# Performance work log

Measured on AMD Instinct MI355X. Metric: run time of the kernel, lower is better.

Reference implementation:

```python
import jax, jax.numpy as jnp
import numpy as np

NEG_SLOPE = 0.2  # PyG GATv2Conv default
TOPK = 10        # hard-coded in original forward


def setup_inputs() -> dict:
    key = jax.random.key(0)
    N, E, D, L = 50000, 640000, 128, 3
    ks = jax.random.split(key, 12)
    s = 1.0 / np.sqrt(D)
    x = jax.random.normal(ks[0], (N, D), jnp.float32)
    edge_index = jax.random.randint(ks[1], (2, E), 0, N, dtype=jnp.int64)
    edge_attributes = jax.random.normal(ks[2], (E, D), jnp.float32)
    # GATv2 per-layer params (heads=1): lin_l (src), lin_r (dst), lin_edge, att, out bias
    Wl = jax.random.normal(ks[3], (L, D, D), jnp.float32) * s
    bl = jnp.zeros((L, D), jnp.float32)
    Wr = jax.random.normal(ks[4], (L, D, D), jnp.float32) * s
    br = jnp.zeros((L, D), jnp.float32)
    We = jax.random.normal(ks[5], (L, D, D), jnp.float32) * s
    att = jax.random.normal(ks[6], (L, D), jnp.float32) * s
    bias = jnp.zeros((L, D), jnp.float32)
    # final Conv1d(D, 1, 1) == linear projection D -> 1 per node
    Wf = jax.random.normal(ks[7], (D, 1), jnp.float32) * s
    bf = jnp.zeros((1,), jnp.float32)
    return {"x": x, "edge_index": edge_index, "edge_attributes": edge_attributes,
            "Wl": Wl, "bl": bl, "Wr": Wr, "br": br, "We": We, "att": att,
            "bias": bias, "Wf": Wf, "bf": bf}


def _gatv2_layer(x, src, dst, ea, N, Wl, bl, Wr, br, We, att, bias):
    xl = x @ Wl + bl            # [N, D] source transform
    xr = x @ Wr + br            # [N, D] target transform
    ee = ea @ We                # [E', D] edge transform (no bias in PyG lin_edge)
    m = jax.nn.leaky_relu(xl[src] + xr[dst] + ee, NEG_SLOPE)  # [E', D]
    logits = m @ att            # [E']
    # per-destination softmax (every node has a self-loop -> no empty segments)
    mx = jax.ops.segment_max(logits, dst, num_segments=N)
    w = jnp.exp(logits - mx[dst])
    den = jax.ops.segment_sum(w, dst, num_segments=N)
    alpha = w / den[dst]
    out = jax.ops.segment_sum(xl[src] * alpha[:, None], dst, num_segments=N)
    return out + bias


def reference(x, edge_index, edge_attributes, Wl, bl, Wr, br, We, att, bias, Wf, bf):
    N, D = x.shape
    src, dst = edge_index[0], edge_index[1]
    loop = jnp.arange(N, dtype=src.dtype)
    # add_self_loops with fill_value='mean': loop attr = mean of incoming edge attrs
    cnt = jax.ops.segment_sum(jnp.ones_like(dst, dtype=x.dtype), dst, num_segments=N)
    loop_attr = jax.ops.segment_sum(edge_attributes, dst, num_segments=N) / jnp.maximum(cnt, 1.0)[:, None]
    src_f = jnp.concatenate([src, loop])
    dst_f = jnp.concatenate([dst, loop])
    ea = jnp.concatenate([edge_attributes, loop_attr], axis=0)
    L = Wl.shape[0]
    for i in range(L):
        x = _gatv2_layer(x, src_f, dst_f, ea, N, Wl[i], bl[i], Wr[i], br[i], We[i], att[i], bias[i])
    scores = (x @ Wf)[:, 0] + bf[0]   # Conv1d(D,1,1): per-node scalar score [N]
    vals, idx = jax.lax.top_k(scores, TOPK)
    return vals, idx
```

## Files before the change

### kernel.cpp

```cpp
#include <hip/hip_runtime.h>
#include <hip/hip_bf16.h>
#include <float.h>

#define DD 128
#define NEG_SLOPE 0.2f
#define TKB 128

typedef __attribute__((ext_vector_type(8))) short bf16x8;
typedef __attribute__((ext_vector_type(4))) float f32x4;

__device__ __forceinline__ float lrelu(float v) {
    return fmaxf(v, 0.0f) + NEG_SLOPE * fminf(v, 0.0f);
}

__device__ __forceinline__ unsigned short f2bf(float f) {
    unsigned u = __float_as_uint(f);
    u += 0x7fff + ((u >> 16) & 1);
    return (unsigned short)(u >> 16);
}
__device__ __forceinline__ float bf2f(unsigned short h) {
    return __uint_as_float(((unsigned)h) << 16);
}


__global__ void k_hist(const int* __restrict__ dst, int E, int* __restrict__ cnt) {
    int i = blockIdx.x * blockDim.x + threadIdx.x;
    if (i < E) atomicAdd(&cnt[dst[i]], 1);
}

__global__ __launch_bounds__(1024) void k_scan(const int* __restrict__ cnt,
                                               int* __restrict__ row_ptr, int N) {
    __shared__ int sums[1024];
    int tid = threadIdx.x;
    int total = N + 1;
    int chunk = (total + 1023) / 1024;
    int lo = tid * chunk;
    int hi = min(lo + chunk, total);
    int s = 0;
    for (int i = lo; i < hi; ++i) s += (i < N) ? (cnt[i] + 1) : 0;
    sums[tid] = s;
    __syncthreads();
    for (int off = 1; off < 1024; off <<= 1) {
        int t = (tid >= off) ? sums[tid - off] : 0;
        __syncthreads();
        sums[tid] += t;
        __syncthreads();
    }
    int run = sums[tid] - s;
    for (int i = lo; i < hi; ++i) {
        row_ptr[i] = run;
        run += (i < N) ? (cnt[i] + 1) : 0;
    }
}

__global__ void k_scatter(const int* __restrict__ dst, int E, int N,
                          const int* __restrict__ row_ptr, int* __restrict__ fill,
                          const int* __restrict__ cnt, int* __restrict__ eids) {
    int i = blockIdx.x * blockDim.x + threadIdx.x;
    int tot = E + N;
    if (i >= tot) return;
    if (i < E) {
        int d = dst[i];
        int p = atomicAdd(&fill[d], 1);
        eids[row_ptr[d] + p] = i;
    } else {
        int n = i - E;
        eids[row_ptr[n] + cnt[n]] = E + n;
    }
}

__global__ void k_sort_rows(const int* __restrict__ row_ptr, int* __restrict__ eids, int N) {
    int n = blockIdx.x * blockDim.x + threadIdx.x;
    if (n >= N) return;
    int s = row_ptr[n], e = row_ptr[n + 1];
    for (int i = s + 1; i < e; ++i) {
        int v = eids[i];
        int j = i - 1;
        while (j >= s && eids[j] > v) { eids[j + 1] = eids[j]; --j; }
        eids[j + 1] = v;
    }
}

__global__ void k_invert(const int* __restrict__ eids, const int* __restrict__ srcArr,
                         int* __restrict__ pos, int* __restrict__ csr_src, int Etot, int E) {
    int p = blockIdx.x * blockDim.x + threadIdx.x;
    if (p >= Etot) return;
    int eid = eids[p];
    pos[eid] = p;
    csr_src[p] = (eid < E) ? srcArr[eid] : (eid - E);
}

__global__ __launch_bounds__(256) void k_ea_pack(const float* __restrict__ ea,
                                                 const int* __restrict__ row_ptr,
                                                 const int* __restrict__ cnt,
                                                 const int* __restrict__ eids,
                                                 unsigned short* __restrict__ eh,
                                                 unsigned short* __restrict__ el,
                                                 int N, int E) {
    int wid = (blockIdx.x * blockDim.x + threadIdx.x) >> 6;
    int lane = threadIdx.x & 63;
    if (wid >= N) return;
    int s = row_ptr[wid];
    int c = cnt[wid];
    float2 acc = make_float2(0.f, 0.f);
    for (int c0 = 0; c0 < c; c0 += 64) {
        int m = min(64, c - c0);
        int eid = 0;
        if (lane < m) eid = eids[s + c0 + lane];
        int p = 0;
        for (; p + 2 <= m; p += 2) {
            int e0 = __shfl(eid, p), e1 = __shfl(eid, p + 1);
            float2 v0 = *reinterpret_cast<const float2*>(ea + (size_t)e0 * DD + 2 * lane);
            float2 v1 = *reinterpret_cast<const float2*>(ea + (size_t)e1 * DD + 2 * lane);
            acc.x += v0.x; acc.y += v0.y;
            acc.x += v1.x; acc.y += v1.y;
            ushort2 h0, l0, h1, l1;
            h0.x = f2bf(v0.x); l0.x = f2bf(v0.x - bf2f(h0.x));
            h0.y = f2bf(v0.y); l0.y = f2bf(v0.y - bf2f(h0.y));
            h1.x = f2bf(v1.x); l1.x = f2bf(v1.x - bf2f(h1.x));
            h1.y = f2bf(v1.y); l1.y = f2bf(v1.y - bf2f(h1.y));
            *reinterpret_cast<ushort2*>(eh + (size_t)e0 * DD + 2 * lane) = h0;
            *reinterpret_cast<ushort2*>(el + (size_t)e0 * DD + 2 * lane) = l0;
            *reinterpret_cast<ushort2*>(eh + (size_t)e1 * DD + 2 * lane) = h1;
            *reinterpret_cast<ushort2*>(el + (size_t)e1 * DD + 2 * lane) = l1;
        }
        for (; p < m; ++p) {
            int e = __shfl(eid, p);
            float2 v = *reinterpret_cast<const float2*>(ea + (size_t)e * DD + 2 * lane);
            acc.x += v.x; acc.y += v.y;
            ushort2 h, l;
            h.x = f2bf(v.x); l.x = f2bf(v.x - bf2f(h.x));
            h.y = f2bf(v.y); l.y = f2bf(v.y - bf2f(h.y));
            *reinterpret_cast<ushort2*>(eh + (size_t)e * DD + 2 * lane) = h;
            *reinterpret_cast<ushort2*>(el + (size_t)e * DD + 2 * lane) = l;
        }
    }
    float inv = 1.0f / fmaxf((float)c, 1.0f);
    float2 o = make_float2(acc.x * inv, acc.y * inv);
    ushort2 h, l;
    h.x = f2bf(o.x); l.x = f2bf(o.x - bf2f(h.x));
    h.y = f2bf(o.y); l.y = f2bf(o.y - bf2f(h.y));
    *reinterpret_cast<ushort2*>(eh + (size_t)(E + wid) * DD + 2 * lane) = h;
    *reinterpret_cast<ushort2*>(el + (size_t)(E + wid) * DD + 2 * lane) = l;
}

__global__ void k_prepack(const float* __restrict__ W, unsigned short* __restrict__ WA, int L) {
    int idx = blockIdx.x * blockDim.x + threadIdx.x;
    int total = L * DD * DD;
    if (idx >= total) return;
    int l = idx >> 14;
    int rem = idx & 16383;
    int k = rem >> 7;
    int j = rem & 127;
    float w = W[(size_t)l * 16384 + (size_t)k * DD + j];
    unsigned short h = f2bf(w);
    unsigned short lo = f2bf(w - bf2f(h));
    int ks = k >> 5, g = (k >> 3) & 3, i = k & 7;
    size_t off = ((size_t)(ks * 4 + g) * DD + j) * 8 + i;
    unsigned short* base = WA + (size_t)l * 32768;
    base[off] = h;
    base[16384 + off] = lo;
}


__global__ __launch_bounds__(512) void k_gemm2(
    const float* __restrict__ X,
    const unsigned short* __restrict__ WAl, const unsigned short* __restrict__ WAr,
    const float* __restrict__ bl, const float* __restrict__ br,
    float* __restrict__ Yl, float* __restrict__ Yr, int N) {

    __shared__ unsigned short WAs[65536];
    {
        const uint4* g1 = reinterpret_cast<const uint4*>(WAl);
        const uint4* g2 = reinterpret_cast<const uint4*>(WAr);
        uint4* l1 = reinterpret_cast<uint4*>(WAs);
        uint4* l2 = reinterpret_cast<uint4*>(WAs + 32768);
        int t = threadIdx.x;
        #pragma unroll
        for (int i = 0; i < 8; ++i) {
            l1[t + i * 512] = g1[t + i * 512];
            l2[t + i * 512] = g2[t + i * 512];
        }
    }
    __syncthreads();

    int tid  = threadIdx.x;
    int lane = tid & 63;
    int wv   = tid >> 6;
    int lc   = lane & 15;
    int g    = lane >> 4;

    int r0 = blockIdx.x * 256 + wv * 32;
    int rv[2]; bool ok[2];
    const float* rp[2];
    #pragma unroll
    for (int nf = 0; nf < 2; ++nf) {
        rv[nf] = r0 + nf * 16 + lc;
        ok[nf] = (rv[nf] < N);
        rp[nf] = X + (size_t)(ok[nf] ? rv[nf] : 0) * DD;
    }

    f32x4 accl[8][2], accr[8][2];
    #pragma unroll
    for (int m = 0; m < 8; ++m)
        #pragma unroll
        for (int n = 0; n < 2; ++n) {
            accl[m][n] = (f32x4){0.f, 0.f, 0.f, 0.f};
            accr[m][n] = (f32x4){0.f, 0.f, 0.f, 0.f};
        }

    float4 pr0[2], pr1[2];
    #pragma unroll
    for (int nf = 0; nf < 2; ++nf) {
        pr0[nf] = *reinterpret_cast<const float4*>(rp[nf] + g * 8);
        pr1[nf] = *reinterpret_cast<const float4*>(rp[nf] + g * 8 + 4);
    }

    #pragma unroll
    for (int ks = 0; ks < 4; ++ks) {
        bf16x8 Bh[2], Bl[2];
        #pragma unroll
        for (int nf = 0; nf < 2; ++nf) {
            float v[8] = {pr0[nf].x, pr0[nf].y, pr0[nf].z, pr0[nf].w,
                          pr1[nf].x, pr1[nf].y, pr1[nf].z, pr1[nf].w};
            #pragma unroll
            for (int i = 0; i < 8; ++i) {
                unsigned short h = f2bf(v[i]);
                Bh[nf][i] = (short)h;
                Bl[nf][i] = (short)f2bf(v[i] - bf2f(h));
            }
        }
        if (ks < 3) {
            int k0n = (ks + 1) * 32 + g * 8;
            #pragma unroll
            for (int nf = 0; nf < 2; ++nf) {
                pr0[nf] = *reinterpret_cast<const float4*>(rp[nf] + k0n);
                pr1[nf] = *reinterpret_cast<const float4*>(rp[nf] + k0n + 4);
            }
        }
        #pragma unroll
        for (int mf = 0; mf < 8; ++mf) {
            int aoff = ((ks * 4 + g) * DD + (mf * 16 + lc)) * 8;
            bf16x8 Ahl = *reinterpret_cast<const bf16x8*>(&WAs[aoff]);
            bf16x8 All = *reinterpret_cast<const bf16x8*>(&WAs[16384 + aoff]);
            bf16x8 Ahr = *reinterpret_cast<const bf16x8*>(&WAs[32768 + aoff]);
            bf16x8 Alr = *reinterpret_cast<const bf16x8*>(&WAs[49152 + aoff]);
            #pragma unroll
            for (int nf = 0; nf < 2; ++nf) {
                accl[mf][nf] = __builtin_amdgcn_mfma_f32_16x16x32_bf16(Ahl, Bh[nf], accl[mf][nf], 0, 0, 0);
                accl[mf][nf] = __builtin_amdgcn_mfma_f32_16x16x32_bf16(All, Bh[nf], accl[mf][nf], 0, 0, 0);
                accl[mf][nf] = __builtin_amdgcn_mfma_f32_16x16x32_bf16(Ahl, Bl[nf], accl[mf][nf], 0, 0, 0);
                accr[mf][nf] = __builtin_amdgcn_mfma_f32_16x16x32_bf16(Ahr, Bh[nf], accr[mf][nf], 0, 0, 0);
                accr[mf][nf] = __builtin_amdgcn_mfma_f32_16x16x32_bf16(Alr, Bh[nf], accr[mf][nf], 0, 0, 0);
                accr[mf][nf] = __builtin_amdgcn_mfma_f32_16x16x32_bf16(Ahr, Bl[nf], accr[mf][nf], 0, 0, 0);
            }
        }
    }

    #pragma unroll
    for (int mf = 0; mf < 8; ++mf) {
        int f0 = mf * 16 + g * 4;
        float4 blv = *reinterpret_cast<const float4*>(bl + f0);
        float4 brv = *reinterpret_cast<const float4*>(br + f0);
        #pragma unroll
        for (int nf = 0; nf < 2; ++nf) {
            if (!ok[nf]) continue;
            float4 o;
            o.x = accl[mf][nf][0] + blv.x;
            o.y = accl[mf][nf][1] + blv.y;
            o.z = accl[mf][nf][2] + blv.z;
            o.w = accl[mf][nf][3] + blv.w;
            *reinterpret_cast<float4*>(Yl + (size_t)rv[nf] * DD + f0) = o;
            o.x = accr[mf][nf][0] + brv.x;
            o.y = accr[mf][nf][1] + brv.y;
            o.z = accr[mf][nf][2] + brv.z;
            o.w = accr[mf][nf][3] + brv.w;
            *reinterpret_cast<float4*>(Yr + (size_t)rv[nf] * DD + f0) = o;
        }
    }
}

__global__ __launch_bounds__(512, 4) void k_edge_mfma(
    const unsigned short* __restrict__ eh, const unsigned short* __restrict__ el,
    const int* __restrict__ srcArr, const int* __restrict__ dstArr,
    const unsigned short* __restrict__ WA, const float* __restrict__ att,
    const float* __restrict__ xl, const float* __restrict__ xr,
    const int* __restrict__ pos, float* __restrict__ wlog, int E, int Etot) {

    __shared__ unsigned short WAs[32768];
    {
        const uint4* gsrc = reinterpret_cast<const uint4*>(WA);
        uint4* ldst = reinterpret_cast<uint4*>(WAs);
        int t = threadIdx.x;
        #pragma unroll
        for (int i = 0; i < 8; ++i) ldst[t + i * 512] = gsrc[t + i * 512];
    }
    __syncthreads();

    int tid  = threadIdx.x;
    int lane = tid & 63;
    int wv   = tid >> 6;
    int lc   = lane & 15;
    int g    = lane >> 4;

    int e = blockIdx.x * 128 + wv * 16 + lc;
    bool ok = (e < Etot);
    int er = ok ? e : 0;
    const unsigned short* bhp = eh + (size_t)er * DD;
    const unsigned short* blp = el + (size_t)er * DD;

    f32x4 acc[8];
    #pragma unroll
    for (int m = 0; m < 8; ++m) acc[m] = (f32x4){0.f, 0.f, 0.f, 0.f};

    #pragma unroll
    for (int ks = 0; ks < 4; ++ks) {
        int k0 = ks * 32 + g * 8;
        bf16x8 Bh = *reinterpret_cast<const bf16x8*>(bhp + k0);
        bf16x8 Bl = *reinterpret_cast<const bf16x8*>(blp + k0);
        #pragma unroll
        for (int mf = 0; mf < 8; ++mf) {
            int aoff = ((ks * 4 + g) * DD + (mf * 16 + lc)) * 8;
            bf16x8 Ah = *reinterpret_cast<const bf16x8*>(&WAs[aoff]);
            bf16x8 Al = *reinterpret_cast<const bf16x8*>(&WAs[16384 + aoff]);
            acc[mf] = __builtin_amdgcn_mfma_f32_16x16x32_bf16(Ah, Bh, acc[mf], 0, 0, 0);
            acc[mf] = __builtin_amdgcn_mfma_f32_16x16x32_bf16(Al, Bh, acc[mf], 0, 0, 0);
            acc[mf] = __builtin_amdgcn_mfma_f32_16x16x32_bf16(Ah, Bl, acc[mf], 0, 0, 0);
        }
    }

    int sn, dn;
    if (e < E)  { sn = srcArr[e]; dn = dstArr[e]; }
    else if (ok){ sn = e - E; dn = e - E; }
    else        { sn = 0; dn = 0; }
    float partial = 0.f;
    #pragma unroll
    for (int mf = 0; mf < 8; ++mf) {
        int f0 = mf * 16 + g * 4;
        float4 attv = *reinterpret_cast<const float4*>(att + f0);
        float4 xlv  = *reinterpret_cast<const float4*>(xl + (size_t)sn * DD + f0);
        float4 xrv  = *reinterpret_cast<const float4*>(xr + (size_t)dn * DD + f0);
        float t0 = acc[mf][0] + xlv.x + xrv.x;
        float t1 = acc[mf][1] + xlv.y + xrv.y;
        float t2 = acc[mf][2] + xlv.z + xrv.z;
        float t3 = acc[mf][3] + xlv.w + xrv.w;
        partial += attv.x * lrelu(t0) + attv.y * lrelu(t1)
                 + attv.z * lrelu(t2) + attv.w * lrelu(t3);
    }
    partial += __shfl_xor(partial, 16);
    partial += __shfl_xor(partial, 32);
    if (lane < 16 && ok) wlog[pos[e]] = partial;
}

__global__ __launch_bounds__(256) void k_sfx_agg(
    const float* __restrict__ wlog, const int* __restrict__ row_ptr,
    const int* __restrict__ csr_src, const float* __restrict__ xl,
    const float* __restrict__ bias, float* __restrict__ xout, int N) {
    int wid = (blockIdx.x * blockDim.x + threadIdx.x) >> 6;
    int lane = threadIdx.x & 63;
    if (wid >= N) return;
    int s = row_ptr[wid], e = row_ptr[wid + 1];
    float mx = -FLT_MAX;
    for (int c0 = s; c0 < e; c0 += 64) {
        float l = (c0 + lane < e) ? wlog[c0 + lane] : -FLT_MAX;
        l = fmaxf(l, __shfl_xor(l, 32));
        l = fmaxf(l, __shfl_xor(l, 16));
        l = fmaxf(l, __shfl_xor(l, 8));
        l = fmaxf(l, __shfl_xor(l, 4));
        l = fmaxf(l, __shfl_xor(l, 2));
        l = fmaxf(l, __shfl_xor(l, 1));
        mx = fmaxf(mx, l);
    }
    float den = 0.f;
    for (int c0 = s; c0 < e; c0 += 64) {
        float w = (c0 + lane < e) ? __expf(wlog[c0 + lane] - mx) : 0.f;
        w += __shfl_xor(w, 32);
        w += __shfl_xor(w, 16);
        w += __shfl_xor(w, 8);
        w += __shfl_xor(w, 4);
        w += __shfl_xor(w, 2);
        w += __shfl_xor(w, 1);
        den += w;
    }
    float inv = 1.0f / den;
    float2 acc = make_float2(0.f, 0.f);
    for (int c0 = s; c0 < e; c0 += 64) {
        int m = min(64, e - c0);
        float av = 0.f; int sv = 0;
        if (lane < m) {
            av = __expf(wlog[c0 + lane] - mx) * inv;
            sv = csr_src[c0 + lane];
        }
        int p = 0;
        for (; p + 4 <= m; p += 4) {
            float a0 = __shfl(av, p),     a1 = __shfl(av, p + 1);
            float a2 = __shfl(av, p + 2), a3 = __shfl(av, p + 3);
            int   r0 = __shfl(sv, p),     r1 = __shfl(sv, p + 1);
            int   r2 = __shfl(sv, p + 2), r3 = __shfl(sv, p + 3);
            float2 v0 = *reinterpret_cast<const float2*>(xl + (size_t)r0 * DD + 2 * lane);
            float2 v1 = *reinterpret_cast<const float2*>(xl + (size_t)r1 * DD + 2 * lane);
            float2 v2 = *reinterpret_cast<const float2*>(xl + (size_t)r2 * DD + 2 * lane);
            float2 v3 = *reinterpret_cast<const float2*>(xl + (size_t)r3 * DD + 2 * lane);
            acc.x += a0 * v0.x; acc.y += a0 * v0.y;
            acc.x += a1 * v1.x; acc.y += a1 * v1.y;
            acc.x += a2 * v2.x; acc.y += a2 * v2.y;
            acc.x += a3 * v3.x; acc.y += a3 * v3.y;
        }
        for (; p < m; ++p) {
            float ap = __shfl(av, p);
            int   rw = __shfl(sv, p);
            float2 v = *reinterpret_cast<const float2*>(xl + (size_t)rw * DD + 2 * lane);
            acc.x += ap * v.x;
            acc.y += ap * v.y;
        }
    }
    float2 bv = *reinterpret_cast<const float2*>(bias + 2 * lane);
    float2 o = make_float2(acc.x + bv.x, acc.y + bv.y);
    *reinterpret_cast<float2*>(xout + (size_t)wid * DD + 2 * lane) = o;
}


__global__ __launch_bounds__(256) void k_scores(const float* __restrict__ X,
                                                const float* __restrict__ Wf,
                                                const float* __restrict__ bf,
                                                float* __restrict__ scores, int N) {
    int gid = blockIdx.x * blockDim.x + threadIdx.x;
    int node = gid >> 6;
    int lane = threadIdx.x & 63;
    if (node >= N) return;
    float2 xv = *reinterpret_cast<const float2*>(&X[(size_t)node * DD + lane * 2]);
    float2 wv = *reinterpret_cast<const float2*>(&Wf[lane * 2]);
    float p = xv.x * wv.x + xv.y * wv.y;
    p += __shfl_xor(p, 32);
    p += __shfl_xor(p, 16);
    p += __shfl_xor(p, 8);
    p += __shfl_xor(p, 4);
    p += __shfl_xor(p, 2);
    p += __shfl_xor(p, 1);
    if (lane == 0) scores[node] = p + bf[0];
}

__device__ __forceinline__ bool tk_better(float a, int ai, float b, int bi) {
    return (a > b) || (a == b && ai < bi);
}

__device__ __forceinline__ void tk_insert(float sv, int si, float* v, int* ix) {
    if (tk_better(sv, si, v[9], ix[9])) {
        v[9] = sv; ix[9] = si;
        #pragma unroll
        for (int j = 9; j > 0; --j) {
            if (tk_better(v[j], ix[j], v[j - 1], ix[j - 1])) {
                float tv = v[j]; v[j] = v[j - 1]; v[j - 1] = tv;
                int ti = ix[j]; ix[j] = ix[j - 1]; ix[j - 1] = ti;
            }
        }
    }
}

__global__ __launch_bounds__(256) void k_topk1(const float* __restrict__ scores, int N,
                                               float* __restrict__ cand_v, int* __restrict__ cand_i) {
    __shared__ float lv[256 * 10];
    __shared__ int li[256 * 10];
    int t = threadIdx.x;
    float v[10]; int ix[10];
    #pragma unroll
    for (int j = 0; j < 10; ++j) { v[j] = -FLT_MAX; ix[j] = 0x7fffffff; }
    for (int i = blockIdx.x * 256 + t; i < N; i += TKB * 256)
        tk_insert(scores[i], i, v, ix);
    #pragma unroll
    for (int j = 0; j < 10; ++j) { lv[t * 10 + j] = v[j]; li[t * 10 + j] = ix[j]; }
    __syncthreads();
    for (int sh = 128; sh >= 1; sh >>= 1) {
        if (t < sh) {
            float bv[10]; int bi[10];
            #pragma unroll
            for (int j = 0; j < 10; ++j) { bv[j] = lv[(t + sh) * 10 + j]; bi[j] = li[(t + sh) * 10 + j]; }
            float mv[10]; int mi[10];
            int i1 = 0, i2 = 0;
            #pragma unroll
            for (int k = 0; k < 10; ++k) {
                if (tk_better(v[i1], ix[i1], bv[i2], bi[i2])) { mv[k] = v[i1]; mi[k] = ix[i1]; ++i1; }
                else { mv[k] = bv[i2]; mi[k] = bi[i2]; ++i2; }
            }
            #pragma unroll
            for (int j = 0; j < 10; ++j) {
                v[j] = mv[j]; ix[j] = mi[j];
                lv[t * 10 + j] = v[j]; li[t * 10 + j] = ix[j];
            }
        }
        __syncthreads();
    }
    if (t == 0) {
        #pragma unroll
        for (int j = 0; j < 10; ++j) {
            cand_v[blockIdx.x * 10 + j] = v[j];
            cand_i[blockIdx.x * 10 + j] = ix[j];
        }
    }
}

__global__ __launch_bounds__(64) void k_topk2(const float* __restrict__ cand_v,
                                              const int* __restrict__ cand_i,
                                              float* __restrict__ out) {
    __shared__ float lv[64 * 10];
    __shared__ int li[64 * 10];
    int t = threadIdx.x;
    float v[10]; int ix[10];
    #pragma unroll
    for (int j = 0; j < 10; ++j) { v[j] = -FLT_MAX; ix[j] = 0x7fffffff; }
    for (int i = t; i < TKB * 10; i += 64)
        tk_insert(cand_v[i], cand_i[i], v, ix);
    #pragma unroll
    for (int j = 0; j < 10; ++j) { lv[t * 10 + j] = v[j]; li[t * 10 + j] = ix[j]; }
    __syncthreads();
    for (int sh = 32; sh >= 1; sh >>= 1) {
        if (t < sh) {
            float bv[10]; int bi[10];
            #pragma unroll
            for (int j = 0; j < 10; ++j) { bv[j] = lv[(t + sh) * 10 + j]; bi[j] = li[(t + sh) * 10 + j]; }
            float mv[10]; int mi[10];
            int i1 = 0, i2 = 0;
            #pragma unroll
            for (int k = 0; k < 10; ++k) {
                if (tk_better(v[i1], ix[i1], bv[i2], bi[i2])) { mv[k] = v[i1]; mi[k] = ix[i1]; ++i1; }
                else { mv[k] = bv[i2]; mi[k] = bi[i2]; ++i2; }
            }
            #pragma unroll
            for (int j = 0; j < 10; ++j) {
                v[j] = mv[j]; ix[j] = mi[j];
                lv[t * 10 + j] = v[j]; li[t * 10 + j] = ix[j];
            }
        }
        __syncthreads();
    }
    if (t == 0) {
        #pragma unroll
        for (int j = 0; j < 10; ++j) {
            out[j] = v[j];
            out[10 + j] = (float)ix[j];
        }
    }
}


static inline size_t alignup(size_t v) { return (v + 255) & ~(size_t)255; }

extern "C" void kernel_launch(void* const* d_in, const int* in_sizes, int n_in,
                              void* d_out, int out_size, void* d_ws, size_t ws_size,
                              hipStream_t stream) {
    const float* x    = (const float*)d_in[0];
    const int*   ei   = (const int*)d_in[1];
    const float* ea   = (const float*)d_in[2];
    const float* Wl   = (const float*)d_in[3];
    const float* bl   = (const float*)d_in[4];
    const float* Wr   = (const float*)d_in[5];
    const float* br   = (const float*)d_in[6];
    const float* We   = (const float*)d_in[7];
    const float* att  = (const float*)d_in[8];
    const float* bias = (const float*)d_in[9];
    const float* Wf   = (const float*)d_in[10];
    const float* bf   = (const float*)d_in[11];

    int N = in_sizes[0] / DD;
    int E = in_sizes[1] / 2;
    int L = in_sizes[3] / (DD * DD);
    int Etot = E + N;
    const int* src = ei;
    const int* dst = ei + E;

    size_t off = 0;
    char* wsb = (char*)d_ws;
    auto carve = [&](size_t bytes) -> void* { void* p = wsb + off; off += alignup(bytes); return p; };
    unsigned short* WAe = (unsigned short*)carve((size_t)L * 32768 * 2);
    unsigned short* WAl = (unsigned short*)carve((size_t)L * 32768 * 2);
    unsigned short* WAr = (unsigned short*)carve((size_t)L * 32768 * 2);
    int*   cnt       = (int*)carve((size_t)N * 4);
    int*   fill      = (int*)carve((size_t)N * 4);
    int*   row_ptr   = (int*)carve((size_t)(N + 1) * 4);
    int*   eids      = (int*)carve((size_t)Etot * 4);
    int*   pos       = (int*)carve((size_t)Etot * 4);
    int*   csr_src   = (int*)carve((size_t)Etot * 4);
    float* wlog      = (float*)carve((size_t)Etot * 4);
    unsigned short* eh = (unsigned short*)carve((size_t)Etot * DD * 2);
    unsigned short* el = (unsigned short*)carve((size_t)Etot * DD * 2);
    float* xl        = (float*)carve((size_t)N * DD * 4);
    float* xr        = (float*)carve((size_t)N * DD * 4);
    float* xa        = (float*)carve((size_t)N * DD * 4);
    float* xb        = (float*)carve((size_t)N * DD * 4);
    float* scoresBuf = (float*)carve((size_t)N * 4);
    float* cand_v    = (float*)carve((size_t)TKB * 10 * 4);
    int*   cand_i    = (int*)carve((size_t)TKB * 10 * 4);
    (void)ws_size; (void)n_in; (void)out_size;

    hipMemsetAsync(cnt, 0, (size_t)N * 4, stream);
    hipMemsetAsync(fill, 0, (size_t)N * 4, stream);

    int ppBlocks = (L * DD * DD + 255) / 256;
    k_prepack<<<ppBlocks, 256, 0, stream>>>(We, WAe, L);
    k_prepack<<<ppBlocks, 256, 0, stream>>>(Wl, WAl, L);
    k_prepack<<<ppBlocks, 256, 0, stream>>>(Wr, WAr, L);
    k_hist<<<(E + 255) / 256, 256, 0, stream>>>(dst, E, cnt);
    k_scan<<<1, 1024, 0, stream>>>(cnt, row_ptr, N);
    k_scatter<<<(Etot + 255) / 256, 256, 0, stream>>>(dst, E, N, row_ptr, fill, cnt, eids);
    k_sort_rows<<<(N + 255) / 256, 256, 0, stream>>>(row_ptr, eids, N);
    k_invert<<<(Etot + 255) / 256, 256, 0, stream>>>(eids, src, pos, csr_src, Etot, E);
    int waveBlocks = (N * 64 + 255) / 256;
    k_ea_pack<<<waveBlocks, 256, 0, stream>>>(ea, row_ptr, cnt, eids, eh, el, N, E);

    const float* xin = x;
    float* xout = xa;
    int gemmBlocks = (N + 255) / 256;
    int edgeBlocks = (Etot + 127) / 128;
    for (int l = 0; l < L; ++l) {
        k_gemm2<<<gemmBlocks, 512, 0, stream>>>(xin, WAl + (size_t)l * 32768, WAr + (size_t)l * 32768,
                                                bl + (size_t)l * DD, br + (size_t)l * DD, xl, xr, N);
        k_edge_mfma<<<edgeBlocks, 512, 0, stream>>>(eh, el, src, dst,
                                                    WAe + (size_t)l * 32768, att + (size_t)l * DD,
                                                    xl, xr, pos, wlog, E, Etot);
        k_sfx_agg<<<waveBlocks, 256, 0, stream>>>(wlog, row_ptr, csr_src, xl,
                                                  bias + (size_t)l * DD, xout, N);
        xin = xout;
        xout = (xout == xa) ? xb : xa;
    }
    k_scores<<<(N + 3) / 4, 256, 0, stream>>>(xin, Wf, bf, scoresBuf, N);
    k_topk1<<<TKB, 256, 0, stream>>>(scoresBuf, N, cand_v, cand_i);
    k_topk2<<<1, 64, 0, stream>>>(cand_v, cand_i, (float*)d_out);
}
```

Measured before the change: 1.284 ms.

## Fuse edge logit MFMA, online softmax, and aggregation into per-node kernel

Edge attributes are now stored in CSR (destination-sorted) order, so each wave can process one destination node's incoming edges in chunks of 16. The edge-transform MFMA, logit, online softmax and weighted aggregation of xl all happen in one persistent kernel. This drops the wlog and pos buffers and the separate softmax/aggregate pass. The cost is wasted MFMA lanes when a node has fewer than 16 edges (about 13 on average here), many shuffles per chunk for the reduction, and lower occupancy from the new launch bounds.

```diff
diff --git a/kernel.cpp b/kernel.cpp
--- a/kernel.cpp
+++ b/kernel.cpp
@@ -81,12 +81,11 @@
     }
 }
 
-__global__ void k_invert(const int* __restrict__ eids, const int* __restrict__ srcArr,
-                         int* __restrict__ pos, int* __restrict__ csr_src, int Etot, int E) {
+__global__ void k_srcmap(const int* __restrict__ eids, const int* __restrict__ srcArr,
+                         int* __restrict__ csr_src, int Etot, int E) {
     int p = blockIdx.x * blockDim.x + threadIdx.x;
     if (p >= Etot) return;
     int eid = eids[p];
-    pos[eid] = p;
     csr_src[p] = (eid < E) ? srcArr[eid] : (eid - E);
 }
 
@@ -96,7 +95,7 @@
                                                  const int* __restrict__ eids,
                                                  unsigned short* __restrict__ eh,
                                                  unsigned short* __restrict__ el,
-                                                 int N, int E) {
+                                                 int N) {
     int wid = (blockIdx.x * blockDim.x + threadIdx.x) >> 6;
     int lane = threadIdx.x & 63;
     if (wid >= N) return;
@@ -104,11 +103,11 @@
     int c = cnt[wid];
     float2 acc = make_float2(0.f, 0.f);
     for (int c0 = 0; c0 < c; c0 += 64) {
-        int m = min(64, c - c0);
+        int mm = min(64, c - c0);
         int eid = 0;
-        if (lane < m) eid = eids[s + c0 + lane];
+        if (lane < mm) eid = eids[s + c0 + lane];
         int p = 0;
-        for (; p + 2 <= m; p += 2) {
+        for (; p + 2 <= mm; p += 2) {
             int e0 = __shfl(eid, p), e1 = __shfl(eid, p + 1);
             float2 v0 = *reinterpret_cast<const float2*>(ea + (size_t)e0 * DD + 2 * lane);
             float2 v1 = *reinterpret_cast<const float2*>(ea + (size_t)e1 * DD + 2 * lane);
@@ -119,20 +118,23 @@
             h0.y = f2bf(v0.y); l0.y = f2bf(v0.y - bf2f(h0.y));
             h1.x = f2bf(v1.x); l1.x = f2bf(v1.x - bf2f(h1.x));
             h1.y = f2bf(v1.y); l1.y = f2bf(v1.y - bf2f(h1.y));
-            *reinterpret_cast<ushort2*>(eh + (size_t)e0 * DD + 2 * lane) = h0;
-            *reinterpret_cast<ushort2*>(el + (size_t)e0 * DD + 2 * lane) = l0;
-            *reinterpret_cast<ushort2*>(eh + (size_t)e1 * DD + 2 * lane) = h1;
-            *reinterpret_cast<ushort2*>(el + (size_t)e1 * DD + 2 * lane) = l1;
-        }
-        for (; p < m; ++p) {
+            size_t r0 = (size_t)(s + c0 + p) * DD + 2 * lane;
+            size_t r1 = (size_t)(s + c0 + p + 1) * DD + 2 * lane;
+            *reinterpret_cast<ushort2*>(eh + r0) = h0;
+            *reinterpret_cast<ushort2*>(el + r0) = l0;
+            *reinterpret_cast<ushort2*>(eh + r1) = h1;
+            *reinterpret_cast<ushort2*>(el + r1) = l1;
+        }
+        for (; p < mm; ++p) {
             int e = __shfl(eid, p);
             float2 v = *reinterpret_cast<const float2*>(ea + (size_t)e * DD + 2 * lane);
             acc.x += v.x; acc.y += v.y;
             ushort2 h, l;
             h.x = f2bf(v.x); l.x = f2bf(v.x - bf2f(h.x));
             h.y = f2bf(v.y); l.y = f2bf(v.y - bf2f(h.y));
-            *reinterpret_cast<ushort2*>(eh + (size_t)e * DD + 2 * lane) = h;
-            *reinterpret_cast<ushort2*>(el + (size_t)e * DD + 2 * lane) = l;
+            size_t ro = (size_t)(s + c0 + p) * DD + 2 * lane;
+            *reinterpret_cast<ushort2*>(eh + ro) = h;
+            *reinterpret_cast<ushort2*>(el + ro) = l;
         }
     }
     float inv = 1.0f / fmaxf((float)c, 1.0f);
@@ -140,8 +142,9 @@
     ushort2 h, l;
     h.x = f2bf(o.x); l.x = f2bf(o.x - bf2f(h.x));
     h.y = f2bf(o.y); l.y = f2bf(o.y - bf2f(h.y));
-    *reinterpret_cast<ushort2*>(eh + (size_t)(E + wid) * DD + 2 * lane) = h;
-    *reinterpret_cast<ushort2*>(el + (size_t)(E + wid) * DD + 2 * lane) = l;
+    size_t ro = (size_t)(s + c) * DD + 2 * lane;
+    *reinterpret_cast<ushort2*>(eh + ro) = h;
+    *reinterpret_cast<ushort2*>(el + ro) = l;
 }
 
 __global__ void k_prepack(const float* __restrict__ W, unsigned short* __restrict__ WA, int L) {
@@ -280,12 +283,13 @@
     }
 }
 
-__global__ __launch_bounds__(512, 4) void k_edge_mfma(
+__global__ __launch_bounds__(512, 2) void k_node_fused(
     const unsigned short* __restrict__ eh, const unsigned short* __restrict__ el,
-    const int* __restrict__ srcArr, const int* __restrict__ dstArr,
+    const int* __restrict__ row_ptr, const int* __restrict__ csr_src,
     const unsigned short* __restrict__ WA, const float* __restrict__ att,
     const float* __restrict__ xl, const float* __restrict__ xr,
-    const int* __restrict__ pos, float* __restrict__ wlog, int E, int Etot) {
+    const float* __restrict__ bias, float* __restrict__ xout,
+    int N, int nodeStride) {
 
     __shared__ unsigned short WAs[32768];
     {
@@ -303,120 +307,113 @@
     int lc   = lane & 15;
     int g    = lane >> 4;
 
-    int e = blockIdx.x * 128 + wv * 16 + lc;
-    bool ok = (e < Etot);
-    int er = ok ? e : 0;
-    const unsigned short* bhp = eh + (size_t)er * DD;
-    const unsigned short* blp = el + (size_t)er * DD;
-
-    f32x4 acc[8];
-    #pragma unroll
-    for (int m = 0; m < 8; ++m) acc[m] = (f32x4){0.f, 0.f, 0.f, 0.f};
-
-    #pragma unroll
-    for (int ks = 0; ks < 4; ++ks) {
-        int k0 = ks * 32 + g * 8;
-        bf16x8 Bh = *reinterpret_cast<const bf16x8*>(bhp + k0);
-        bf16x8 Bl = *reinterpret_cast<const bf16x8*>(blp + k0);
-        #pragma unroll
-        for (int mf = 0; mf < 8; ++mf) {
-            int aoff = ((ks * 4 + g) * DD + (mf * 16 + lc)) * 8;
-            bf16x8 Ah = *reinterpret_cast<const bf16x8*>(&WAs[aoff]);
-            bf16x8 Al = *reinterpret_cast<const bf16x8*>(&WAs[16384 + aoff]);
-            acc[mf] = __builtin_amdgcn_mfma_f32_16x16x32_bf16(Ah, Bh, acc[mf], 0, 0, 0);
-            acc[mf] = __builtin_amdgcn_mfma_f32_16x16x32_bf16(Al, Bh, acc[mf], 0, 0, 0);
-            acc[mf] = __builtin_amdgcn_mfma_f32_16x16x32_bf16(Ah, Bl, acc[mf], 0, 0, 0);
-        }
-    }
-
-    int sn, dn;
-    if (e < E)  { sn = srcArr[e]; dn = dstArr[e]; }
-    else if (ok){ sn = e - E; dn = e - E; }
-    else        { sn = 0; dn = 0; }
-    float partial = 0.f;
-    #pragma unroll
-    for (int mf = 0; mf < 8; ++mf) {
-        int f0 = mf * 16 + g * 4;
-        float4 attv = *reinterpret_cast<const float4*>(att + f0);
-        float4 xlv  = *reinterpret_cast<const float4*>(xl + (size_t)sn * DD + f0);
-        float4 xrv  = *reinterpret_cast<const float4*>(xr + (size_t)dn * DD + f0);
-        float t0 = acc[mf][0] + xlv.x + xrv.x;
-        float t1 = acc[mf][1] + xlv.y + xrv.y;
-        float t2 = acc[mf][2] + xlv.z + xrv.z;
-        float t3 = acc[mf][3] + xlv.w + xrv.w;
-        partial += attv.x * lrelu(t0) + attv.y * lrelu(t1)
-                 + attv.z * lrelu(t2) + attv.w * lrelu(t3);
-    }
-    partial += __shfl_xor(partial, 16);
-    partial += __shfl_xor(partial, 32);
-    if (lane < 16 && ok) wlog[pos[e]] = partial;
-}
-
-__global__ __launch_bounds__(256) void k_sfx_agg(
-    const float* __restrict__ wlog, const int* __restrict__ row_ptr,
-    const int* __restrict__ csr_src, const float* __restrict__ xl,
-    const float* __restrict__ bias, float* __restrict__ xout, int N) {
-    int wid = (blockIdx.x * blockDim.x + threadIdx.x) >> 6;
-    int lane = threadIdx.x & 63;
-    if (wid >= N) return;
-    int s = row_ptr[wid], e = row_ptr[wid + 1];
-    float mx = -FLT_MAX;
-    for (int c0 = s; c0 < e; c0 += 64) {
-        float l = (c0 + lane < e) ? wlog[c0 + lane] : -FLT_MAX;
-        l = fmaxf(l, __shfl_xor(l, 32));
-        l = fmaxf(l, __shfl_xor(l, 16));
-        l = fmaxf(l, __shfl_xor(l, 8));
-        l = fmaxf(l, __shfl_xor(l, 4));
-        l = fmaxf(l, __shfl_xor(l, 2));
-        l = fmaxf(l, __shfl_xor(l, 1));
-        mx = fmaxf(mx, l);
-    }
-    float den = 0.f;
-    for (int c0 = s; c0 < e; c0 += 64) {
-        float w = (c0 + lane < e) ? __expf(wlog[c0 + lane] - mx) : 0.f;
-        w += __shfl_xor(w, 32);
-        w += __shfl_xor(w, 16);
-        w += __shfl_xor(w, 8);
-        w += __shfl_xor(w, 4);
-        w += __shfl_xor(w, 2);
-        w += __shfl_xor(w, 1);
-        den += w;
-    }
-    float inv = 1.0f / den;
-    float2 acc = make_float2(0.f, 0.f);
-    for (int c0 = s; c0 < e; c0 += 64) {
-        int m = min(64, e - c0);
-        float av = 0.f; int sv = 0;
-        if (lane < m) {
-            av = __expf(wlog[c0 + lane] - mx) * inv;
-            sv = csr_src[c0 + lane];
-        }
-        int p = 0;
-        for (; p + 4 <= m; p += 4) {
-            float a0 = __shfl(av, p),     a1 = __shfl(av, p + 1);
-            float a2 = __shfl(av, p + 2), a3 = __shfl(av, p + 3);
-            int   r0 = __shfl(sv, p),     r1 = __shfl(sv, p + 1);
-            int   r2 = __shfl(sv, p + 2), r3 = __shfl(sv, p + 3);
-            float2 v0 = *reinterpret_cast<const float2*>(xl + (size_t)r0 * DD + 2 * lane);
-            float2 v1 = *reinterpret_cast<const float2*>(xl + (size_t)r1 * DD + 2 * lane);
-            float2 v2 = *reinterpret_cast<const float2*>(xl + (size_t)r2 * DD + 2 * lane);
-            float2 v3 = *reinterpret_cast<const float2*>(xl + (size_t)r3 * DD + 2 * lane);
-            acc.x += a0 * v0.x; acc.y += a0 * v0.y;
-            acc.x += a1 * v1.x; acc.y += a1 * v1.y;
-            acc.x += a2 * v2.x; acc.y += a2 * v2.y;
-            acc.x += a3 * v3.x; acc.y += a3 * v3.y;
-        }
-        for (; p < m; ++p) {
-            float ap = __shfl(av, p);
-            int   rw = __shfl(sv, p);
-            float2 v = *reinterpret_cast<const float2*>(xl + (size_t)rw * DD + 2 * lane);
-            acc.x += ap * v.x;
-            acc.y += ap * v.y;
-        }
-    }
-    float2 bv = *reinterpret_cast<const float2*>(bias + 2 * lane);
-    float2 o = make_float2(acc.x + bv.x, acc.y + bv.y);
-    *reinterpret_cast<float2*>(xout + (size_t)wid * DD + 2 * lane) = o;
+    for (int n = blockIdx.x * 8 + wv; n < N; n += nodeStride) {
+        int s = row_ptr[n], e = row_ptr[n + 1];
+        float m = -FLT_MAX, den = 0.f;
+        f32x4 outv[8];
+        #pragma unroll
+        for (int mf = 0; mf < 8; ++mf) outv[mf] = (f32x4){0.f, 0.f, 0.f, 0.f};
+
+        for (int c0 = s; c0 < e; c0 += 16) {
+            int slot = c0 + lc;
+            bool valid = (slot < e);
+            int sl = valid ? slot : s;
+            const unsigned short* bhp = eh + (size_t)sl * DD;
+            const unsigned short* blp = el + (size_t)sl * DD;
+
+            f32x4 acc[8];
+            #pragma unroll
+            for (int mf = 0; mf < 8; ++mf) acc[mf] = (f32x4){0.f, 0.f, 0.f, 0.f};
+
+            #pragma unroll
+            for (int ks = 0; ks < 4; ++ks) {
+                int k0 = ks * 32 + g * 8;
+                bf16x8 Bh = *reinterpret_cast<const bf16x8*>(bhp + k0);
+                bf16x8 Bl = *reinterpret_cast<const bf16x8*>(blp + k0);
+                #pragma unroll
+                for (int mf = 0; mf < 8; ++mf) {
+                    int aoff = ((ks * 4 + g) * DD + (mf * 16 + lc)) * 8;
+                    bf16x8 Ah = *reinterpret_cast<const bf16x8*>(&WAs[aoff]);
+                    bf16x8 Al = *reinterpret_cast<const bf16x8*>(&WAs[16384 + aoff]);
+                    acc[mf] = __builtin_amdgcn_mfma_f32_16x16x32_bf16(Ah, Bh, acc[mf], 0, 0, 0);
+                    acc[mf] = __builtin_amdgcn_mfma_f32_16x16x32_bf16(Al, Bh, acc[mf], 0, 0, 0);
+                    acc[mf] = __builtin_amdgcn_mfma_f32_16x16x32_bf16(Ah, Bl, acc[mf], 0, 0, 0);
+                }
+            }
+
+            int src = csr_src[sl];
+            float partial = 0.f;
+            f32x4 v[8];
+            #pragma unroll
+            for (int mf = 0; mf < 8; ++mf) {
+                int f0 = mf * 16 + g * 4;
+                float4 attv = *reinterpret_cast<const float4*>(att + f0);
+                float4 xlv  = *reinterpret_cast<const float4*>(xl + (size_t)src * DD + f0);
+                float4 xrv  = *reinterpret_cast<const float4*>(xr + (size_t)n   * DD + f0);
+                float t0 = acc[mf][0] + xlv.x + xrv.x;
+                float t1 = acc[mf][1] + xlv.y + xrv.y;
+                float t2 = acc[mf][2] + xlv.z + xrv.z;
+                float t3 = acc[mf][3] + xlv.w + xrv.w;
+                partial += attv.x * lrelu(t0) + attv.y * lrelu(t1)
+                         + attv.z * lrelu(t2) + attv.w * lrelu(t3);
+                v[mf] = (f32x4){xlv.x, xlv.y, xlv.z, xlv.w};
+            }
+            partial += __shfl_xor(partial, 16);
+            partial += __shfl_xor(partial, 32);
+            float logit = valid ? partial : -FLT_MAX;
+
+            float cm = logit;
+            cm = fmaxf(cm, __shfl_xor(cm, 1));
+            cm = fmaxf(cm, __shfl_xor(cm, 2));
+            cm = fmaxf(cm, __shfl_xor(cm, 4));
+            cm = fmaxf(cm, __shfl_xor(cm, 8));
+            float mn = fmaxf(m, cm);
+            float scale = __expf(m - mn);
+            float alpha = valid ? __expf(logit - mn) : 0.f;
+            float asum = alpha;
+            asum += __shfl_xor(asum, 1);
+            asum += __shfl_xor(asum, 2);
+            asum += __shfl_xor(asum, 4);
+            asum += __shfl_xor(asum, 8);
+            den = den * scale + asum;
+            m = mn;
+
+            #pragma unroll
+            for (int mf = 0; mf < 8; ++mf) {
+                float w0 = v[mf][0] * alpha;
+                float w1 = v[mf][1] * alpha;
+                float w2 = v[mf][2] * alpha;
+                float w3 = v[mf][3] * alpha;
+                w0 += __shfl_xor(w0, 1); w1 += __shfl_xor(w1, 1);
+                w2 += __shfl_xor(w2, 1); w3 += __shfl_xor(w3, 1);
+                w0 += __shfl_xor(w0, 2); w1 += __shfl_xor(w1, 2);
+                w2 += __shfl_xor(w2, 2); w3 += __shfl_xor(w3, 2);
+                w0 += __shfl_xor(w0, 4); w1 += __shfl_xor(w1, 4);
+                w2 += __shfl_xor(w2, 4); w3 += __shfl_xor(w3, 4);
+                w0 += __shfl_xor(w0, 8); w1 += __shfl_xor(w1, 8);
+                w2 += __shfl_xor(w2, 8); w3 += __shfl_xor(w3, 8);
+                outv[mf][0] = outv[mf][0] * scale + w0;
+                outv[mf][1] = outv[mf][1] * scale + w1;
+                outv[mf][2] = outv[mf][2] * scale + w2;
+                outv[mf][3] = outv[mf][3] * scale + w3;
+            }
+        }
+
+        float invden = 1.0f / den;
+        if (lc == 0) {
+            #pragma unroll
+            for (int mf = 0; mf < 8; ++mf) {
+                int f0 = mf * 16 + g * 4;
+                float4 bv = *reinterpret_cast<const float4*>(bias + f0);
+                float4 o;
+                o.x = outv[mf][0] * invden + bv.x;
+                o.y = outv[mf][1] * invden + bv.y;
+                o.z = outv[mf][2] * invden + bv.z;
+                o.w = outv[mf][3] * invden + bv.w;
+                *reinterpret_cast<float4*>(xout + (size_t)n * DD + f0) = o;
+            }
+        }
+    }
 }
 
 
@@ -578,9 +575,7 @@
     int*   fill      = (int*)carve((size_t)N * 4);
     int*   row_ptr   = (int*)carve((size_t)(N + 1) * 4);
     int*   eids      = (int*)carve((size_t)Etot * 4);
-    int*   pos       = (int*)carve((size_t)Etot * 4);
     int*   csr_src   = (int*)carve((size_t)Etot * 4);
-    float* wlog      = (float*)carve((size_t)Etot * 4);
     unsigned short* eh = (unsigned short*)carve((size_t)Etot * DD * 2);
     unsigned short* el = (unsigned short*)carve((size_t)Etot * DD * 2);
     float* xl        = (float*)carve((size_t)N * DD * 4);
@@ -603,22 +598,22 @@
     k_scan<<<1, 1024, 0, stream>>>(cnt, row_ptr, N);
     k_scatter<<<(Etot + 255) / 256, 256, 0, stream>>>(dst, E, N, row_ptr, fill, cnt, eids);
     k_sort_rows<<<(N + 255) / 256, 256, 0, stream>>>(row_ptr, eids, N);
-    k_invert<<<(Etot + 255) / 256, 256, 0, stream>>>(eids, src, pos, csr_src, Etot, E);
+    k_srcmap<<<(Etot + 255) / 256, 256, 0, stream>>>(eids, src, csr_src, Etot, E);
     int waveBlocks = (N * 64 + 255) / 256;
-    k_ea_pack<<<waveBlocks, 256, 0, stream>>>(ea, row_ptr, cnt, eids, eh, el, N, E);
+    k_ea_pack<<<waveBlocks, 256, 0, stream>>>(ea, row_ptr, cnt, eids, eh, el, N);
 
     const float* xin = x;
     float* xout = xa;
     int gemmBlocks = (N + 255) / 256;
-    int edgeBlocks = (Etot + 127) / 128;
+    int fusedBlocks = 1024;
+    int nodeStride = fusedBlocks * 8;
     for (int l = 0; l < L; ++l) {
         k_gemm2<<<gemmBlocks, 512, 0, stream>>>(xin, WAl + (size_t)l * 32768, WAr + (size_t)l * 32768,
                                                 bl + (size_t)l * DD, br + (size_t)l * DD, xl, xr, N);
-        k_edge_mfma<<<edgeBlocks, 512, 0, stream>>>(eh, el, src, dst,
-                                                    WAe + (size_t)l * 32768, att + (size_t)l * DD,
-                                                    xl, xr, pos, wlog, E, Etot);
-        k_sfx_agg<<<waveBlocks, 256, 0, stream>>>(wlog, row_ptr, csr_src, xl,
-                                                  bias + (size_t)l * DD, xout, N);
+        k_node_fused<<<fusedBlocks, 512, 0, stream>>>(eh, el, row_ptr, csr_src,
+                                                      WAe + (size_t)l * 32768, att + (size_t)l * DD,
+                                                      xl, xr, bias + (size_t)l * DD, xout,
+                                                      N, nodeStride);
         xin = xout;
         xout = (xout == xa) ? xb : xa;
     }
```

New measurement: 5.079 ms. +295.5%, slower.
